# Kernel optimization log

Hardware: AMD Instinct MI355X
Metric: run time of the kernel (lower is better)

Reference implementation:

```python
import jax, jax.numpy as jnp
import numpy as np

EPS = 1e-5  # nn.LayerNorm default

def _ln(x, g, b):
    m = x.mean(-1, keepdims=True)
    v = ((x - m) ** 2).mean(-1, keepdims=True)
    return (x - m) / jnp.sqrt(v + EPS) * g + b


def setup_inputs() -> dict:
    key = jax.random.key(0)
    ks = jax.random.split(key, 16)
    B, T, H, W = 8, 20, 224, 224
    D, NC = 1536, 7
    s = 0.02
    f32 = jnp.float32
    return {
        'x': jax.random.normal(ks[0], (B, 3, T, H, W), f32),
        'timestamp': jax.random.uniform(ks[1], (B,), f32),
        # surrogate backbone: patchify conv (stride 16) + global avg pool -> 1536 feats
        'conv_w': jax.random.normal(ks[2], (D, 3, 16, 16), f32) * s,
        'conv_b': jnp.zeros((D,), f32),
        'w_red': jax.random.normal(ks[3], (D, D), f32) * s,
        'b_red': jnp.zeros((D,), f32),
        'w_num': jax.random.normal(ks[4], (D, 1), f32) * s,
        'b_num': jnp.zeros((D,), f32),
        'time_embed': jax.random.normal(ks[5], (1, T, D), f32) * s,
        'cls_swap': jax.random.normal(ks[6], (1, 5, 1, D), f32) * s,
        'ln_g': jnp.ones((D,), f32),
        'ln_b': jnp.zeros((D,), f32),
        'w_qkv': jax.random.normal(ks[7], (3 * D, D), f32) * s,
        'w_tproj': jax.random.normal(ks[8], (D, D), f32) * s,
        'b_tproj': jnp.zeros((D,), f32),
        'w_tfc': jax.random.normal(ks[9], (D, D), f32) * s,
        'b_tfc': jnp.zeros((D,), f32),
        'w_head': jax.random.normal(ks[10], (NC, D), f32) * s,
        'b_head': jnp.zeros((NC,), f32),
    }


def reference(x, timestamp, conv_w, conv_b, w_red, b_red, w_num, b_num,
              time_embed, cls_swap, ln_g, ln_b, w_qkv, w_tproj, b_tproj,
              w_tfc, b_tfc, w_head, b_head):
    B, C, T, H, W = x.shape
    D = w_red.shape[0]
    NH = 12
    HD = D // NH
    scale = HD ** -0.5

    # (b t) c h w  -> backbone surrogate -> (B*T, D)
    xf = jnp.transpose(x, (0, 2, 1, 3, 4)).reshape(B * T, C, H, W)
    f = jax.lax.conv_general_dilated(
        xf, conv_w, window_strides=(16, 16), padding='VALID',
        dimension_numbers=('NCHW', 'OIHW', 'NCHW'))
    f = (f + conv_b[None, :, None, None]).mean((2, 3))  # global avg pool -> (BT, D)

    xr = (f @ w_red.T + b_red).reshape(B, T, D)           # reduce_dim
    xt = xr + time_embed
    te = timestamp[:, None] @ w_num.T + b_num             # NumberToVector (B, D)
    xt = xt + te[:, None, :]

    # groups: b (n k) c -> b n k c, k=4, n=5; prepend 1 cls token per group
    g = jnp.concatenate(
        [jnp.broadcast_to(cls_swap, (B, 5, 1, D)), xt.reshape(B, 5, 4, D)], axis=2)

    for _ in range(4):  # num_interactions
        gr = g.reshape(B * 5, 5, D)
        hn = _ln(gr, ln_g, ln_b)
        qkv = (hn @ w_qkv.T).reshape(B * 5, 5, 3, NH, HD).transpose(2, 0, 3, 1, 4)
        q, k, v = qkv[0], qkv[1], qkv[2]                  # (b*n, h, t, hd)
        a = jax.nn.softmax(jnp.einsum('bhqd,bhkd->bhqk', q, k) * scale, axis=-1)
        o = jnp.einsum('bhqk,bhkd->bhqd', a, v).transpose(0, 2, 1, 3).reshape(B * 5, 5, D)
        o = o @ w_tproj.T + b_tproj                       # attn proj
        upd = (o @ w_tfc.T + b_tfc) + gr                  # temporal_fc + residual
        g = upd.reshape(B, 5, 5, D)
        # swap cls tokens between groups via roll
        g = g.at[:, :, 0, :].set(jnp.roll(g[:, :, 0, :], 1, axis=1))

    xt = g[:, :, 1:, :].reshape(B, T, D)
    out = xt[:, -1, :] + xr[:, -1, :]
    return out @ w_head.T + b_head  # (B, num_classes)
```

## Files before the change

### kernel.cpp

```cpp
#include <hip/hip_runtime.h>

typedef __attribute__((ext_vector_type(8))) short short8;
typedef __attribute__((ext_vector_type(8))) unsigned short ushort8;
typedef __attribute__((ext_vector_type(4))) float f32x4;
typedef unsigned short ushort_t;

__device__ __forceinline__ ushort_t f2bf(float f) {
    unsigned u = __builtin_bit_cast(unsigned, f);
    u += 0x7fffu + ((u >> 16) & 1u);
    return (ushort_t)(u >> 16);
}
__device__ __forceinline__ float bf2f(ushort_t u) {
    unsigned v = ((unsigned)u) << 16;
    return __builtin_bit_cast(float, v);
}

__device__ __forceinline__ void load_lds16(const void* gp, void* lp) {
    __builtin_amdgcn_global_load_lds(
        (const __attribute__((address_space(1))) void*)gp,
        (__attribute__((address_space(3))) void*)lp, 16, 0, 0);
}

__global__ __launch_bounds__(256, 4) void pool_kernel(
    const float* __restrict__ x, ushort_t* __restrict__ AP) {
    int blk = blockIdx.x, tid = threadIdx.x;
    int bt = blk / 12, rc = blk % 12;
    int c = rc >> 2, igrp = rc & 3;
    int w = tid >> 6, lane = tid & 63;
    int i = igrp * 4 + w;
    int b = bt / 20, t = bt % 20;
    const float* base = x + (size_t)((b * 3 + c) * 20 + t) * 50176;

    f32x4 v[13];
    #pragma unroll
    for (int it = 0; it < 13; ++it) {
        int k = lane + it * 64;
        int kk = k < 784 ? k : 0;
        int ri = (kk * 9363) >> 19;
        int c4 = kk - ri * 56;
        v[it] = *(const f32x4*)(base + (16 * ri + i) * 224 + 4 * c4);
        if (k >= 784) v[it] = (f32x4){0.f, 0.f, 0.f, 0.f};
    }
    #pragma unroll
    for (int s = 1; s < 13; s <<= 1)
        #pragma unroll
        for (int j = 0; j + s < 13; j += 2 * s)
            v[j] += v[j + s];
    f32x4 acc = v[0];
    #pragma unroll
    for (int m = 4; m <= 32; m <<= 1) {
        acc[0] += __shfl_xor(acc[0], m);
        acc[1] += __shfl_xor(acc[1], m);
        acc[2] += __shfl_xor(acc[2], m);
        acc[3] += __shfl_xor(acc[3], m);
    }
    if (lane < 4) {
        ushort4 o;
        o.x = f2bf(acc[0] * (1.f / 196.f));
        o.y = f2bf(acc[1] * (1.f / 196.f));
        o.z = f2bf(acc[2] * (1.f / 196.f));
        o.w = f2bf(acc[3] * (1.f / 196.f));
        *(ushort4*)(AP + (size_t)bt * 768 + c * 256 + i * 16 + 4 * lane) = o;
    }
}

__global__ __launch_bounds__(256) void wprep_kernel(
    const float* __restrict__ w_qkv, const float* __restrict__ w_tf,
    const float* __restrict__ w_red, const float* __restrict__ conv_w,
    const float* __restrict__ w_tp, const float* __restrict__ b_tp,
    const float* __restrict__ b_tf, const float* __restrict__ cls,
    ushort_t* __restrict__ WQ, ushort_t* __restrict__ WF,
    ushort_t* __restrict__ WR, ushort_t* __restrict__ WCV,
    ushort_t* __restrict__ WTT, float* __restrict__ BC,
    float* __restrict__ GA) {
    __shared__ __align__(16) float smem[64 * 68];
    int blk = blockIdx.x, tid = threadIdx.x;
    if (blk < 6336) {
        long c = (long)blk * 256 + tid;
        const float* s; ushort_t* d; long i;
        if (c < 884736)       { s = w_qkv;  d = WQ;  i = c; }
        else if (c < 1179648) { s = w_tf;   d = WF;  i = c - 884736; }
        else if (c < 1474560) { s = w_red;  d = WR;  i = c - 1179648; }
        else                  { s = conv_w; d = WCV; i = c - 1474560; }
        i <<= 3;
        f32x4 a = *(const f32x4*)(s + i);
        f32x4 b = *(const f32x4*)(s + i + 4);
        ushort8 o;
        o[0] = f2bf(a[0]); o[1] = f2bf(a[1]); o[2] = f2bf(a[2]); o[3] = f2bf(a[3]);
        o[4] = f2bf(b[0]); o[5] = f2bf(b[1]); o[6] = f2bf(b[2]); o[7] = f2bf(b[3]);
        *(ushort8*)(d + i) = o;
    } else if (blk < 6912) {
        int tb = blk - 6336;
        int bi = tb / 24, bj = tb % 24;
        int r0 = (tid >> 4) << 2;
        int c0 = (tid & 15) << 2;
        #pragma unroll
        for (int rr = 0; rr < 4; ++rr) {
            f32x4 v = *(const f32x4*)(w_tp + (size_t)(bi * 64 + r0 + rr) * 1536 + bj * 64 + c0);
            smem[(r0 + rr) * 68 + c0 + 0] = v[0];
            smem[(r0 + rr) * 68 + c0 + 1] = v[1];
            smem[(r0 + rr) * 68 + c0 + 2] = v[2];
            smem[(r0 + rr) * 68 + c0 + 3] = v[3];
        }
        __syncthreads();
        #pragma unroll
        for (int rr = 0; rr < 4; ++rr) {
            int jj = r0 + rr;
            ushort4 o;
            o.x = f2bf(smem[(c0 + 0) * 68 + jj]);
            o.y = f2bf(smem[(c0 + 1) * 68 + jj]);
            o.z = f2bf(smem[(c0 + 2) * 68 + jj]);
            o.w = f2bf(smem[(c0 + 3) * 68 + jj]);
            *(ushort4*)(WTT + (size_t)(bj * 64 + jj) * 1536 + bi * 64 + c0) = o;
        }
    } else if (blk < 6952) {
        int cblk = blk - 6912;
        int b = cblk / 5, n = cblk % 5;
        size_t row = (size_t)(b * 25 + n * 5) * 1536;
        #pragma unroll
        for (int j = 0; j < 6; ++j) {
            int d = tid + j * 256;
            GA[row + d] = cls[n * 1536 + d];
        }
    } else {
        int bb = blk - 6952;
        int row = bb * 16 + (tid >> 4);
        int sub = tid & 15;
        float acc = 0.f;
        for (int j = 0; j < 96; ++j) {
            int k = sub + j * 16;
            acc += w_tf[(size_t)row * 1536 + k] * b_tp[k];
        }
        acc += __shfl_xor(acc, 1); acc += __shfl_xor(acc, 2);
        acc += __shfl_xor(acc, 4); acc += __shfl_xor(acc, 8);
        if (sub == 0) BC[row] = acc + b_tf[row];
    }
}

template <int MT, bool OUT_BF16, bool HAS_BIAS, bool HAS_RES, bool CLS_SWAP,
          bool BUILD_G, bool SPLITK>
__global__ __launch_bounds__(64) void gemm_kernel(
    const ushort_t* __restrict__ A, const ushort_t* __restrict__ B,
    void* __restrict__ Cv, void* __restrict__ Cv2,
    const float* __restrict__ bias, const float* __restrict__ res,
    int M, int N, int K, int KS,
    float* __restrict__ g_out, const float* __restrict__ temb,
    const float* __restrict__ ts, const float* __restrict__ w_num,
    const float* __restrict__ b_num) {
    constexpr int BUFB = MT * 2048 + 8192;
    __shared__ __align__(16) char lds[2 * BUFB];
    const int lane = threadIdx.x;
    const int tn = blockIdx.x;
    int tm = blockIdx.y;
    if (SPLITK) {
        int half = tm >> 2;
        tm &= 3;
        if (half) { A += K; B += K; Cv = Cv2; }
    }

    f32x4 acc[MT][4];
    #pragma unroll
    for (int m = 0; m < MT; ++m)
        #pragma unroll
        for (int n = 0; n < 4; ++n)
            acc[m][n] = (f32x4){0.f, 0.f, 0.f, 0.f};

    const int nK = K >> 6;
    const int rbase = lane >> 3, cc = lane & 7;

    auto stage = [&](int k0, int buf) {
        char* lA = lds + buf * BUFB;
        char* lB = lA + MT * 2048;
        #pragma unroll
        for (int j = 0; j < MT * 2; ++j) {
            int row = j * 8 + rbase;
            int cf = cc ^ (row & 7);
            int ga = tm * (MT * 16) + row; if (ga > M - 1) ga = M - 1;
            load_lds16(A + (size_t)ga * KS + (k0 + cf * 8), lA + j * 1024);
        }
        #pragma unroll
        for (int j = 0; j < 8; ++j) {
            int row = j * 8 + rbase;
            int cf = cc ^ (row & 7);
            load_lds16(B + (size_t)(tn * 64 + row) * KS + (k0 + cf * 8), lB + j * 1024);
        }
    };

    stage(0, 0);
    for (int t = 0; t < nK; ++t) {
        int cur = t & 1;
        if (t + 1 < nK) {
            stage((t + 1) << 6, cur ^ 1);
            if constexpr (MT == 2) asm volatile("s_waitcnt vmcnt(12)" ::: "memory");
            else                   asm volatile("s_waitcnt vmcnt(16)" ::: "memory");
        } else {
            asm volatile("s_waitcnt vmcnt(0)" ::: "memory");
        }
        __builtin_amdgcn_sched_barrier(0);
        const char* lA = lds + cur * BUFB;
        const char* lB = lA + MT * 2048;
        #pragma unroll
        for (int ks = 0; ks < 2; ++ks) {
            short8 av[MT], bv[4];
            const int rlo = lane & 15;
            const int chi = ks * 4 + (lane >> 4);
            #pragma unroll
            for (int m = 0; m < MT; ++m) {
                int r = m * 16 + rlo;
                av[m] = *(const short8*)(lA + r * 128 + ((chi ^ (r & 7)) << 4));
            }
            #pragma unroll
            for (int n = 0; n < 4; ++n) {
                int r = n * 16 + rlo;
                bv[n] = *(const short8*)(lB + r * 128 + ((chi ^ (r & 7)) << 4));
            }
            #pragma unroll
            for (int m = 0; m < MT; ++m)
                #pragma unroll
                for (int n = 0; n < 4; ++n)
                    acc[m][n] = __builtin_amdgcn_mfma_f32_16x16x32_bf16(
                        av[m], bv[n], acc[m][n], 0, 0, 0);
        }
    }

    const int c_l = lane & 15, r_q = (lane >> 4) * 4;
    #pragma unroll
    for (int m = 0; m < MT; ++m) {
        #pragma unroll
        for (int reg = 0; reg < 4; ++reg) {
            int r_ = tm * (MT * 16) + m * 16 + r_q + reg;
            if (r_ < M) {
                int r2 = r_;
                if (CLS_SWAP) {
                    int bb = r_ / 25, rem = r_ % 25;
                    if (rem % 5 == 0) r2 = bb * 25 + ((rem / 5 + 1) % 5) * 5;
                }
                #pragma unroll
                for (int n = 0; n < 4; ++n) {
                    int cc_ = tn * 64 + n * 16 + c_l;
                    float v = acc[m][n][reg];
                    if (HAS_BIAS) v += bias[cc_];
                    if (HAS_RES) v += res[(size_t)r_ * N + cc_];
                    if (OUT_BF16) ((ushort_t*)Cv)[(size_t)r2 * N + cc_] = f2bf(v);
                    else          ((float*)Cv)[(size_t)r2 * N + cc_] = v;
                    if (BUILD_G) {
                        int b = r_ / 20, t = r_ % 20;
                        float gval = v + temb[t * 1536 + cc_] +
                                     ts[b] * w_num[cc_] + b_num[cc_];
                        g_out[(size_t)(b * 25 + (t / 4) * 5 + (t % 4) + 1) * 1536 + cc_] = gval;
                    }
                }
            }
        }
    }
}

__global__ __launch_bounds__(256) void ln_kernel(
    const float* __restrict__ g, const float* __restrict__ gamma,
    const float* __restrict__ beta, ushort_t* __restrict__ hn) {
    int r = blockIdx.x, tid = threadIdx.x;
    const float* x = g + (size_t)r * 1536;
    float v[6], s = 0.f, s2 = 0.f;
    #pragma unroll
    for (int j = 0; j < 6; ++j) {
        v[j] = x[tid + j * 256];
        s += v[j]; s2 += v[j] * v[j];
    }
    #pragma unroll
    for (int m = 1; m < 64; m <<= 1) { s += __shfl_xor(s, m); s2 += __shfl_xor(s2, m); }
    __shared__ float red[8];
    int wid = tid >> 6;
    if ((tid & 63) == 0) { red[wid] = s; red[4 + wid] = s2; }
    __syncthreads();
    s  = red[0] + red[1] + red[2] + red[3];
    s2 = red[4] + red[5] + red[6] + red[7];
    float mean = s * (1.0f / 1536.0f);
    float var  = s2 * (1.0f / 1536.0f) - mean * mean;
    float rstd = rsqrtf(var + 1e-5f);
    #pragma unroll
    for (int j = 0; j < 6; ++j) {
        int d = tid + j * 256;
        float y = (v[j] - mean) * rstd * gamma[d] + beta[d];
        hn[(size_t)r * 1536 + d] = f2bf(y);
    }
}

__global__ __launch_bounds__(64) void attn_kernel(
    const float* __restrict__ qA, const float* __restrict__ qB,
    ushort_t* __restrict__ o) {
    int gid = blockIdx.x;
    int h = gid % 12, gg = gid / 12;
    int l = threadIdx.x;
    size_t off = (size_t)gg * 5 * 4608 + h * 128 + 2 * l;
    const float* b0 = qA + off;
    const float* b1 = qB + off;
    float q[5][2], k[5][2], v[5][2];
    #pragma unroll
    for (int tt = 0; tt < 5; ++tt) {
        float2 q0 = *(const float2*)(b0 + tt * 4608);
        float2 q1 = *(const float2*)(b1 + tt * 4608);
        float2 k0 = *(const float2*)(b0 + tt * 4608 + 1536);
        float2 k1 = *(const float2*)(b1 + tt * 4608 + 1536);
        float2 v0 = *(const float2*)(b0 + tt * 4608 + 3072);
        float2 v1 = *(const float2*)(b1 + tt * 4608 + 3072);
        q[tt][0] = q0.x + q1.x; q[tt][1] = q0.y + q1.y;
        k[tt][0] = k0.x + k1.x; k[tt][1] = k0.y + k1.y;
        v[tt][0] = v0.x + v1.x; v[tt][1] = v0.y + v1.y;
    }
    float sc[5][5];
    #pragma unroll
    for (int i = 0; i < 5; ++i)
        #pragma unroll
        for (int j = 0; j < 5; ++j)
            sc[i][j] = q[i][0] * k[j][0] + q[i][1] * k[j][1];
    #pragma unroll
    for (int m = 1; m < 64; m <<= 1)
        #pragma unroll
        for (int i = 0; i < 5; ++i)
            #pragma unroll
            for (int j = 0; j < 5; ++j)
                sc[i][j] += __shfl_xor(sc[i][j], m);
    const float scale = 0.08838834764831845f;
    float a_[5][5];
    #pragma unroll
    for (int i = 0; i < 5; ++i) {
        float mx = -1e30f;
        #pragma unroll
        for (int j = 0; j < 5; ++j) mx = fmaxf(mx, sc[i][j]);
        float sum = 0.f;
        #pragma unroll
        for (int j = 0; j < 5; ++j) { a_[i][j] = __expf((sc[i][j] - mx) * scale); sum += a_[i][j]; }
        float inv = 1.0f / sum;
        #pragma unroll
        for (int j = 0; j < 5; ++j) a_[i][j] *= inv;
    }
    #pragma unroll
    for (int i = 0; i < 5; ++i) {
        float o0 = 0.f, o1 = 0.f;
        #pragma unroll
        for (int j = 0; j < 5; ++j) { o0 += a_[i][j] * v[j][0]; o1 += a_[i][j] * v[j][1]; }
        ushort2 w; w.x = f2bf(o0); w.y = f2bf(o1);
        *(ushort2*)(o + (size_t)(gg * 5 + i) * 1536 + h * 128 + 2 * l) = w;
    }
}

__global__ __launch_bounds__(64) void head_kernel(
    const float* __restrict__ gfin, const float* __restrict__ xr,
    const float* __restrict__ w_head, const float* __restrict__ b_head,
    float* __restrict__ out) {
    int b = blockIdx.x, l = threadIdx.x;
    const float* gv = gfin + (size_t)(b * 25 + 24) * 1536;
    const float* xv = xr + (size_t)(b * 20 + 19) * 1536;
    float acc[7] = {0, 0, 0, 0, 0, 0, 0};
    for (int d = l; d < 1536; d += 64) {
        float xval = gv[d] + xv[d];
        #pragma unroll
        for (int c = 0; c < 7; ++c) acc[c] += xval * w_head[c * 1536 + d];
    }
    #pragma unroll
    for (int c = 0; c < 7; ++c)
        #pragma unroll
        for (int m = 1; m < 64; m <<= 1) acc[c] += __shfl_xor(acc[c], m);
    if (l == 0) {
        #pragma unroll
        for (int c = 0; c < 7; ++c) out[b * 7 + c] = acc[c] + b_head[c];
    }
}

#define OFF_WQ    0u
#define OFF_WF    14155776u
#define OFF_WR    18874368u
#define OFF_WCV   23592960u
#define OFF_WTT   25952256u
#define OFF_WC    30670848u
#define OFF_BC    35389440u
#define OFF_AP    35395584u
#define OFF_FBF   35641344u
#define OFF_XR    36132864u
#define OFF_GA    37115904u
#define OFF_GB    38344704u
#define OFF_HN    39573504u
#define OFF_QKV0  40187904u
#define OFF_QKV1  43874304u
#define OFF_OBF   47560704u

extern "C" void kernel_launch(void* const* d_in, const int* in_sizes, int n_in,
                              void* d_out, int out_size, void* d_ws, size_t ws_size,
                              hipStream_t stream) {
    const float* x      = (const float*)d_in[0];
    const float* ts     = (const float*)d_in[1];
    const float* conv_w = (const float*)d_in[2];
    const float* conv_b = (const float*)d_in[3];
    const float* w_red  = (const float*)d_in[4];
    const float* b_red  = (const float*)d_in[5];
    const float* w_num  = (const float*)d_in[6];
    const float* b_num  = (const float*)d_in[7];
    const float* temb   = (const float*)d_in[8];
    const float* cls    = (const float*)d_in[9];
    const float* ln_g   = (const float*)d_in[10];
    const float* ln_b   = (const float*)d_in[11];
    const float* w_qkv  = (const float*)d_in[12];
    const float* w_tp   = (const float*)d_in[13];
    const float* b_tp   = (const float*)d_in[14];
    const float* w_tf   = (const float*)d_in[15];
    const float* b_tf   = (const float*)d_in[16];
    const float* w_head = (const float*)d_in[17];
    const float* b_head = (const float*)d_in[18];

    char* ws = (char*)d_ws;
    ushort_t* WQ   = (ushort_t*)(ws + OFF_WQ);
    ushort_t* WF   = (ushort_t*)(ws + OFF_WF);
    ushort_t* WR   = (ushort_t*)(ws + OFF_WR);
    ushort_t* WCV  = (ushort_t*)(ws + OFF_WCV);
    ushort_t* WTT  = (ushort_t*)(ws + OFF_WTT);
    ushort_t* WC   = (ushort_t*)(ws + OFF_WC);
    float*    BC   = (float*)(ws + OFF_BC);
    ushort_t* AP   = (ushort_t*)(ws + OFF_AP);
    ushort_t* FBF  = (ushort_t*)(ws + OFF_FBF);
    float*    XR   = (float*)(ws + OFF_XR);
    float*    GA   = (float*)(ws + OFF_GA);
    float*    GB   = (float*)(ws + OFF_GB);
    ushort_t* HN   = (ushort_t*)(ws + OFF_HN);
    float*    QKV0 = (float*)(ws + OFF_QKV0);
    float*    QKV1 = (float*)(ws + OFF_QKV1);
    ushort_t* OBF  = (ushort_t*)(ws + OFF_OBF);

    pool_kernel<<<1920, 256, 0, stream>>>(x, AP);
    wprep_kernel<<<7048, 256, 0, stream>>>(w_qkv, w_tf, w_red, conv_w, w_tp,
                                           b_tp, b_tf, cls,
                                           WQ, WF, WR, WCV, WTT, BC, GA);
    gemm_kernel<4, true, false, false, false, false, false><<<dim3(24, 24), 64, 0, stream>>>(
        WF, WTT, WC, nullptr, nullptr, nullptr, 1536, 1536, 1536, 1536,
        nullptr, nullptr, nullptr, nullptr, nullptr);
    gemm_kernel<2, true, true, false, false, false, false><<<dim3(24, 5), 64, 0, stream>>>(
        AP, WCV, FBF, nullptr, conv_b, nullptr, 160, 1536, 768, 768,
        nullptr, nullptr, nullptr, nullptr, nullptr);
    gemm_kernel<2, false, true, false, false, true, false><<<dim3(24, 5), 64, 0, stream>>>(
        FBF, WR, XR, nullptr, b_red, nullptr, 160, 1536, 1536, 1536,
        GA, temb, ts, w_num, b_num);

    float* gsrc = GA;
    float* gdst = GB;
    for (int it = 0; it < 4; ++it) {
        ln_kernel<<<200, 256, 0, stream>>>(gsrc, ln_g, ln_b, HN);
        gemm_kernel<4, false, false, false, false, false, true><<<dim3(72, 8), 64, 0, stream>>>(
            HN, WQ, QKV0, QKV1, nullptr, nullptr, 200, 4608, 768, 1536,
            nullptr, nullptr, nullptr, nullptr, nullptr);
        attn_kernel<<<480, 64, 0, stream>>>(QKV0, QKV1, OBF);
        gemm_kernel<2, false, true, true, true, false, false><<<dim3(24, 7), 64, 0, stream>>>(
            OBF, WC, gdst, nullptr, BC, gsrc, 200, 1536, 1536, 1536,
            nullptr, nullptr, nullptr, nullptr, nullptr);
        float* tmp = gsrc; gsrc = gdst; gdst = tmp;
    }
    head_kernel<<<8, 64, 0, stream>>>(gsrc, XR, w_head, b_head, (float*)d_out);
}
```

Baseline: 212.7 us.

## Fold LayerNorm into QKV GEMM via gamma-scaled weights and epilogue row stats

```diff
diff --git a/kernel.cpp b/kernel.cpp
--- a/kernel.cpp
+++ b/kernel.cpp
@@ -10,10 +10,6 @@
     u += 0x7fffu + ((u >> 16) & 1u);
     return (ushort_t)(u >> 16);
 }
-__device__ __forceinline__ float bf2f(ushort_t u) {
-    unsigned v = ((unsigned)u) << 16;
-    return __builtin_bit_cast(float, v);
-}
 
 __device__ __forceinline__ void load_lds16(const void* gp, void* lp) {
     __builtin_amdgcn_global_load_lds(
@@ -21,76 +17,81 @@
         (__attribute__((address_space(3))) void*)lp, 16, 0, 0);
 }
 
-__global__ __launch_bounds__(256, 4) void pool_kernel(
-    const float* __restrict__ x, ushort_t* __restrict__ AP) {
-    int blk = blockIdx.x, tid = threadIdx.x;
-    int bt = blk / 12, rc = blk % 12;
-    int c = rc >> 2, igrp = rc & 3;
-    int w = tid >> 6, lane = tid & 63;
-    int i = igrp * 4 + w;
-    int b = bt / 20, t = bt % 20;
-    const float* base = x + (size_t)((b * 3 + c) * 20 + t) * 50176;
-
-    f32x4 v[13];
-    #pragma unroll
-    for (int it = 0; it < 13; ++it) {
-        int k = lane + it * 64;
-        int kk = k < 784 ? k : 0;
-        int ri = (kk * 9363) >> 19;
-        int c4 = kk - ri * 56;
-        v[it] = *(const f32x4*)(base + (16 * ri + i) * 224 + 4 * c4);
-        if (k >= 784) v[it] = (f32x4){0.f, 0.f, 0.f, 0.f};
-    }
-    #pragma unroll
-    for (int s = 1; s < 13; s <<= 1)
-        #pragma unroll
-        for (int j = 0; j + s < 13; j += 2 * s)
-            v[j] += v[j + s];
-    f32x4 acc = v[0];
-    #pragma unroll
-    for (int m = 4; m <= 32; m <<= 1) {
-        acc[0] += __shfl_xor(acc[0], m);
-        acc[1] += __shfl_xor(acc[1], m);
-        acc[2] += __shfl_xor(acc[2], m);
-        acc[3] += __shfl_xor(acc[3], m);
-    }
-    if (lane < 4) {
-        ushort4 o;
-        o.x = f2bf(acc[0] * (1.f / 196.f));
-        o.y = f2bf(acc[1] * (1.f / 196.f));
-        o.z = f2bf(acc[2] * (1.f / 196.f));
-        o.w = f2bf(acc[3] * (1.f / 196.f));
-        *(ushort4*)(AP + (size_t)bt * 768 + c * 256 + i * 16 + 4 * lane) = o;
-    }
-}
-
-__global__ __launch_bounds__(256) void wprep_kernel(
-    const float* __restrict__ w_qkv, const float* __restrict__ w_tf,
-    const float* __restrict__ w_red, const float* __restrict__ conv_w,
-    const float* __restrict__ w_tp, const float* __restrict__ b_tp,
-    const float* __restrict__ b_tf, const float* __restrict__ cls,
-    ushort_t* __restrict__ WQ, ushort_t* __restrict__ WF,
-    ushort_t* __restrict__ WR, ushort_t* __restrict__ WCV,
-    ushort_t* __restrict__ WTT, float* __restrict__ BC,
-    float* __restrict__ GA) {
+__global__ __launch_bounds__(256, 4) void prep_kernel(
+    const float* __restrict__ x, const float* __restrict__ w_qkv,
+    const float* __restrict__ w_tf, const float* __restrict__ w_red,
+    const float* __restrict__ conv_w, const float* __restrict__ w_tp,
+    const float* __restrict__ b_tp, const float* __restrict__ b_tf,
+    const float* __restrict__ cls, const float* __restrict__ ln_g,
+    const float* __restrict__ ln_b,
+    ushort_t* __restrict__ AP, ushort_t* __restrict__ WQg,
+    ushort_t* __restrict__ WF, ushort_t* __restrict__ WR,
+    ushort_t* __restrict__ WCV, ushort_t* __restrict__ WTT,
+    float* __restrict__ BC, float* __restrict__ GA,
+    ushort_t* __restrict__ GBA, float* __restrict__ U,
+    float* __restrict__ W0, float* __restrict__ ST) {
     __shared__ __align__(16) float smem[64 * 68];
     int blk = blockIdx.x, tid = threadIdx.x;
-    if (blk < 6336) {
-        long c = (long)blk * 256 + tid;
-        const float* s; ushort_t* d; long i;
-        if (c < 884736)       { s = w_qkv;  d = WQ;  i = c; }
+    if (blk < 1920) {
+        int bt = blk / 12, rc = blk % 12;
+        int c = rc >> 2, igrp = rc & 3;
+        int w = tid >> 6, lane = tid & 63;
+        int i = igrp * 4 + w;
+        int b = bt / 20, t = bt % 20;
+        const float* base = x + (size_t)((b * 3 + c) * 20 + t) * 50176;
+        f32x4 v[13];
+        #pragma unroll
+        for (int it = 0; it < 13; ++it) {
+            int k = lane + it * 64;
+            int kk = k < 784 ? k : 0;
+            int ri = (kk * 9363) >> 19;
+            int c4 = kk - ri * 56;
+            v[it] = *(const f32x4*)(base + (16 * ri + i) * 224 + 4 * c4);
+            if (k >= 784) v[it] = (f32x4){0.f, 0.f, 0.f, 0.f};
+        }
+        #pragma unroll
+        for (int s = 1; s < 13; s <<= 1)
+            #pragma unroll
+            for (int j = 0; j + s < 13; j += 2 * s)
+                v[j] += v[j + s];
+        f32x4 acc = v[0];
+        #pragma unroll
+        for (int m = 4; m <= 32; m <<= 1) {
+            acc[0] += __shfl_xor(acc[0], m);
+            acc[1] += __shfl_xor(acc[1], m);
+            acc[2] += __shfl_xor(acc[2], m);
+            acc[3] += __shfl_xor(acc[3], m);
+        }
+        if (lane < 4) {
+            ushort4 o;
+            o.x = f2bf(acc[0] * (1.f / 196.f));
+            o.y = f2bf(acc[1] * (1.f / 196.f));
+            o.z = f2bf(acc[2] * (1.f / 196.f));
+            o.w = f2bf(acc[3] * (1.f / 196.f));
+            *(ushort4*)(AP + (size_t)bt * 768 + c * 256 + i * 16 + 4 * lane) = o;
+        }
+    } else if (blk < 8256) {
+        long c = (long)(blk - 1920) * 256 + tid;
+        const float* s; ushort_t* d; long i; bool gm = false;
+        if (c < 884736)       { s = w_qkv;  d = WQg; i = c; gm = true; }
         else if (c < 1179648) { s = w_tf;   d = WF;  i = c - 884736; }
         else if (c < 1474560) { s = w_red;  d = WR;  i = c - 1179648; }
         else                  { s = conv_w; d = WCV; i = c - 1474560; }
         i <<= 3;
         f32x4 a = *(const f32x4*)(s + i);
         f32x4 b = *(const f32x4*)(s + i + 4);
+        if (gm) {
+            int k = (int)(i % 1536);
+            f32x4 g0 = *(const f32x4*)(ln_g + k);
+            f32x4 g1 = *(const f32x4*)(ln_g + k + 4);
+            a *= g0; b *= g1;
+        }
         ushort8 o;
         o[0] = f2bf(a[0]); o[1] = f2bf(a[1]); o[2] = f2bf(a[2]); o[3] = f2bf(a[3]);
         o[4] = f2bf(b[0]); o[5] = f2bf(b[1]); o[6] = f2bf(b[2]); o[7] = f2bf(b[3]);
         *(ushort8*)(d + i) = o;
-    } else if (blk < 6912) {
-        int tb = blk - 6336;
+    } else if (blk < 8832) {
+        int tb = blk - 8256;
         int bi = tb / 24, bj = tb % 24;
         int r0 = (tid >> 4) << 2;
         int c0 = (tid & 15) << 2;
@@ -113,17 +114,31 @@
             o.w = f2bf(smem[(c0 + 3) * 68 + jj]);
             *(ushort4*)(WTT + (size_t)(bj * 64 + jj) * 1536 + bi * 64 + c0) = o;
         }
-    } else if (blk < 6952) {
-        int cblk = blk - 6912;
+    } else if (blk < 8872) {
+        int cblk = blk - 8832;
         int b = cblk / 5, n = cblk % 5;
-        size_t row = (size_t)(b * 25 + n * 5) * 1536;
+        int grow = b * 25 + n * 5;
+        size_t row = (size_t)grow * 1536;
+        float sv = 0.f, sv2 = 0.f;
         #pragma unroll
         for (int j = 0; j < 6; ++j) {
             int d = tid + j * 256;
-            GA[row + d] = cls[n * 1536 + d];
-        }
-    } else {
-        int bb = blk - 6952;
+            float val = cls[n * 1536 + d];
+            GA[row + d] = val;
+            GBA[row + d] = f2bf(val);
+            sv += val; sv2 += val * val;
+        }
+        #pragma unroll
+        for (int m = 1; m < 64; m <<= 1) { sv += __shfl_xor(sv, m); sv2 += __shfl_xor(sv2, m); }
+        int wid = tid >> 6;
+        if ((tid & 63) == 0) { smem[wid] = sv; smem[4 + wid] = sv2; }
+        __syncthreads();
+        if (tid == 0) {
+            ST[grow * 2]     = smem[0] + smem[1] + smem[2] + smem[3];
+            ST[grow * 2 + 1] = smem[4] + smem[5] + smem[6] + smem[7];
+        }
+    } else if (blk < 8968) {
+        int bb = blk - 8872;
         int row = bb * 16 + (tid >> 4);
         int sub = tid & 15;
         float acc = 0.f;
@@ -134,29 +149,37 @@
         acc += __shfl_xor(acc, 1); acc += __shfl_xor(acc, 2);
         acc += __shfl_xor(acc, 4); acc += __shfl_xor(acc, 8);
         if (sub == 0) BC[row] = acc + b_tf[row];
+    } else {
+        int bb = blk - 8968;
+        int row = bb * 16 + (tid >> 4);
+        int sub = tid & 15;
+        float au = 0.f, aw = 0.f;
+        for (int j = 0; j < 96; ++j) {
+            int k = sub + j * 16;
+            float wv = w_qkv[(size_t)row * 1536 + k];
+            au += wv * ln_g[k];
+            aw += wv * ln_b[k];
+        }
+        au += __shfl_xor(au, 1); au += __shfl_xor(au, 2);
+        au += __shfl_xor(au, 4); au += __shfl_xor(au, 8);
+        aw += __shfl_xor(aw, 1); aw += __shfl_xor(aw, 2);
+        aw += __shfl_xor(aw, 4); aw += __shfl_xor(aw, 8);
+        if (sub == 0) { U[row] = au; W0[row] = aw; }
     }
 }
 
 template <int MT, bool OUT_BF16, bool HAS_BIAS, bool HAS_RES, bool CLS_SWAP,
-          bool BUILD_G, bool SPLITK>
-__global__ __launch_bounds__(64) void gemm_kernel(
+          bool BUILD_G, bool WRITE_BF, bool STATS>
+__device__ __forceinline__ void gemm_tile(
+    char* lds, int lane, int tn, int tm,
     const ushort_t* __restrict__ A, const ushort_t* __restrict__ B,
-    void* __restrict__ Cv, void* __restrict__ Cv2,
-    const float* __restrict__ bias, const float* __restrict__ res,
-    int M, int N, int K, int KS,
+    void* __restrict__ Cv, const float* __restrict__ bias,
+    const float* __restrict__ res, int M, int N, int K, int KS,
+    ushort_t* __restrict__ gbf, float* __restrict__ stats,
     float* __restrict__ g_out, const float* __restrict__ temb,
     const float* __restrict__ ts, const float* __restrict__ w_num,
     const float* __restrict__ b_num) {
     constexpr int BUFB = MT * 2048 + 8192;
-    __shared__ __align__(16) char lds[2 * BUFB];
-    const int lane = threadIdx.x;
-    const int tn = blockIdx.x;
-    int tm = blockIdx.y;
-    if (SPLITK) {
-        int half = tm >> 2;
-        tm &= 3;
-        if (half) { A += K; B += K; Cv = Cv2; }
-    }
 
     f32x4 acc[MT][4];
     #pragma unroll
@@ -235,6 +258,12 @@
                     int bb = r_ / 25, rem = r_ % 25;
                     if (rem % 5 == 0) r2 = bb * 25 + ((rem / 5 + 1) % 5) * 5;
                 }
+                int grow = r2;
+                if (BUILD_G) {
+                    int b = r_ / 20, t = r_ % 20;
+                    grow = b * 25 + (t / 4) * 5 + (t % 4) + 1;
+                }
+                float rp = 0.f, rp2 = 0.f;
                 #pragma unroll
                 for (int n = 0; n < 4; ++n) {
                     int cc_ = tn * 64 + n * 16 + c_l;
@@ -247,7 +276,22 @@
                         int b = r_ / 20, t = r_ % 20;
                         float gval = v + temb[t * 1536 + cc_] +
                                      ts[b] * w_num[cc_] + b_num[cc_];
-                        g_out[(size_t)(b * 25 + (t / 4) * 5 + (t % 4) + 1) * 1536 + cc_] = gval;
+                        g_out[(size_t)grow * 1536 + cc_] = gval;
+                        gbf[(size_t)grow * 1536 + cc_] = f2bf(gval);
+                        rp += gval; rp2 += gval * gval;
+                    } else if (WRITE_BF) {
+                        gbf[(size_t)r2 * N + cc_] = f2bf(v);
+                        rp += v; rp2 += v * v;
+                    }
+                }
+                if (STATS) {
+                    rp  += __shfl_xor(rp, 1);  rp2 += __shfl_xor(rp2, 1);
+                    rp  += __shfl_xor(rp, 2);  rp2 += __shfl_xor(rp2, 2);
+                    rp  += __shfl_xor(rp, 4);  rp2 += __shfl_xor(rp2, 4);
+                    rp  += __shfl_xor(rp, 8);  rp2 += __shfl_xor(rp2, 8);
+                    if (c_l == 0) {
+                        atomicAdd(&stats[grow * 2], rp);
+                        atomicAdd(&stats[grow * 2 + 1], rp2);
                     }
                 }
             }
@@ -255,57 +299,102 @@
     }
 }
 
-__global__ __launch_bounds__(256) void ln_kernel(
-    const float* __restrict__ g, const float* __restrict__ gamma,
-    const float* __restrict__ beta, ushort_t* __restrict__ hn) {
-    int r = blockIdx.x, tid = threadIdx.x;
-    const float* x = g + (size_t)r * 1536;
-    float v[6], s = 0.f, s2 = 0.f;
-    #pragma unroll
-    for (int j = 0; j < 6; ++j) {
-        v[j] = x[tid + j * 256];
-        s += v[j]; s2 += v[j] * v[j];
-    }
-    #pragma unroll
-    for (int m = 1; m < 64; m <<= 1) { s += __shfl_xor(s, m); s2 += __shfl_xor(s2, m); }
-    __shared__ float red[8];
-    int wid = tid >> 6;
-    if ((tid & 63) == 0) { red[wid] = s; red[4 + wid] = s2; }
-    __syncthreads();
-    s  = red[0] + red[1] + red[2] + red[3];
-    s2 = red[4] + red[5] + red[6] + red[7];
-    float mean = s * (1.0f / 1536.0f);
-    float var  = s2 * (1.0f / 1536.0f) - mean * mean;
-    float rstd = rsqrtf(var + 1e-5f);
-    #pragma unroll
-    for (int j = 0; j < 6; ++j) {
-        int d = tid + j * 256;
-        float y = (v[j] - mean) * rstd * gamma[d] + beta[d];
-        hn[(size_t)r * 1536 + d] = f2bf(y);
-    }
+__global__ __launch_bounds__(64) void wcf_kernel(
+    const ushort_t* __restrict__ WF, const ushort_t* __restrict__ WTT,
+    const ushort_t* __restrict__ AP, const ushort_t* __restrict__ WCV,
+    ushort_t* __restrict__ WC, ushort_t* __restrict__ FBF,
+    const float* __restrict__ conv_b) {
+    __shared__ __align__(16) char lds[32768];
+    int task = blockIdx.x, lane = threadIdx.x;
+    if (task < 576)
+        gemm_tile<4, true, false, false, false, false, false, false>(
+            lds, lane, task % 24, task / 24, WF, WTT, WC, nullptr, nullptr,
+            1536, 1536, 1536, 1536, nullptr, nullptr,
+            nullptr, nullptr, nullptr, nullptr, nullptr);
+    else {
+        int t2 = task - 576;
+        gemm_tile<4, true, true, false, false, false, false, false>(
+            lds, lane, t2 % 24, t2 / 24, AP, WCV, FBF, conv_b, nullptr,
+            160, 1536, 768, 768, nullptr, nullptr,
+            nullptr, nullptr, nullptr, nullptr, nullptr);
+    }
+}
+
+__global__ __launch_bounds__(64) void xr_kernel(
+    const ushort_t* __restrict__ FBF, const ushort_t* __restrict__ WR,
+    float* __restrict__ XR, const float* __restrict__ b_red,
+    float* __restrict__ G0, ushort_t* __restrict__ G0B,
+    float* __restrict__ ST0, const float* __restrict__ temb,
+    const float* __restrict__ ts, const float* __restrict__ w_num,
+    const float* __restrict__ b_num) {
+    __shared__ __align__(16) char lds[24576];
+    gemm_tile<2, false, true, false, false, true, false, true>(
+        lds, threadIdx.x, blockIdx.x, blockIdx.y, FBF, WR, XR, b_red, nullptr,
+        160, 1536, 1536, 1536, G0B, ST0, G0, temb, ts, w_num, b_num);
+}
+
+__global__ __launch_bounds__(64) void qkv_kernel(
+    const ushort_t* __restrict__ GBF, const ushort_t* __restrict__ WQg,
+    float* __restrict__ C0, float* __restrict__ C1) {
+    __shared__ __align__(16) char lds[32768];
+    int tn = blockIdx.x, tmh = blockIdx.y;
+    int half = tmh >> 2, tm = tmh & 3;
+    gemm_tile<4, false, false, false, false, false, false, false>(
+        lds, threadIdx.x, tn, tm, GBF + half * 768, WQg + half * 768,
+        half ? C1 : C0, nullptr, nullptr, 200, 4608, 768, 1536,
+        nullptr, nullptr, nullptr, nullptr, nullptr, nullptr, nullptr);
+}
+
+__global__ __launch_bounds__(64) void proj_kernel(
+    const ushort_t* __restrict__ OBF, const ushort_t* __restrict__ WC,
+    float* __restrict__ gdst, const float* __restrict__ BC,
+    const float* __restrict__ gsrc, ushort_t* __restrict__ gbf,
+    float* __restrict__ ST) {
+    __shared__ __align__(16) char lds[24576];
+    gemm_tile<2, false, true, true, true, false, true, true>(
+        lds, threadIdx.x, blockIdx.x, blockIdx.y, OBF, WC, gdst, BC, gsrc,
+        200, 1536, 1536, 1536, gbf, ST,
+        nullptr, nullptr, nullptr, nullptr, nullptr);
 }
 
 __global__ __launch_bounds__(64) void attn_kernel(
     const float* __restrict__ qA, const float* __restrict__ qB,
-    ushort_t* __restrict__ o) {
+    const float* __restrict__ U, const float* __restrict__ W0,
+    const float* __restrict__ ST, ushort_t* __restrict__ o) {
     int gid = blockIdx.x;
     int h = gid % 12, gg = gid / 12;
     int l = threadIdx.x;
-    size_t off = (size_t)gg * 5 * 4608 + h * 128 + 2 * l;
+    int col = h * 128 + 2 * l;
+    size_t off = (size_t)gg * 5 * 4608 + col;
     const float* b0 = qA + off;
     const float* b1 = qB + off;
+    float2 uq = *(const float2*)(U + col);
+    float2 uk = *(const float2*)(U + 1536 + col);
+    float2 uv = *(const float2*)(U + 3072 + col);
+    float2 wq = *(const float2*)(W0 + col);
+    float2 wk = *(const float2*)(W0 + 1536 + col);
+    float2 wv = *(const float2*)(W0 + 3072 + col);
     float q[5][2], k[5][2], v[5][2];
     #pragma unroll
     for (int tt = 0; tt < 5; ++tt) {
+        int gr = gg * 5 + tt;
+        float2 st = *(const float2*)(ST + gr * 2);
+        float mean = st.x * (1.0f / 1536.0f);
+        float var = st.y * (1.0f / 1536.0f) - mean * mean;
+        float s = rsqrtf(var + 1e-5f);
+        float sm = s * mean;
         float2 q0 = *(const float2*)(b0 + tt * 4608);
         float2 q1 = *(const float2*)(b1 + tt * 4608);
         float2 k0 = *(const float2*)(b0 + tt * 4608 + 1536);
         float2 k1 = *(const float2*)(b1 + tt * 4608 + 1536);
         float2 v0 = *(const float2*)(b0 + tt * 4608 + 3072);
         float2 v1 = *(const float2*)(b1 + tt * 4608 + 3072);
-        q[tt][0] = q0.x + q1.x; q[tt][1] = q0.y + q1.y;
-        k[tt][0] = k0.x + k1.x; k[tt][1] = k0.y + k1.y;
-        v[tt][0] = v0.x + v1.x; v[tt][1] = v0.y + v1.y;
+        q[tt][0] = s * (q0.x + q1.x) - sm * uq.x + wq.x;
+        q[tt][1] = s * (q0.y + q1.y) - sm * uq.y + wq.y;
+        k[tt][0] = s * (k0.x + k1.x) - sm * uk.x + wk.x;
+        k[tt][1] = s * (k0.y + k1.y) - sm * uk.y + wk.y;
+        v[tt][0] = s * (v0.x + v1.x) - sm * uv.x + wv.x;
+        v[tt][1] = s * (v0.y + v1.y) - sm * uv.y + wv.y;
     }
     float sc[5][5];
     #pragma unroll
@@ -340,7 +429,7 @@
         #pragma unroll
         for (int j = 0; j < 5; ++j) { o0 += a_[i][j] * v[j][0]; o1 += a_[i][j] * v[j][1]; }
         ushort2 w; w.x = f2bf(o0); w.y = f2bf(o1);
-        *(ushort2*)(o + (size_t)(gg * 5 + i) * 1536 + h * 128 + 2 * l) = w;
+        *(ushort2*)(o + (size_t)(gg * 5 + i) * 1536 + col) = w;
     }
 }
 
@@ -379,10 +468,14 @@
 #define OFF_XR    36132864u
 #define OFF_GA    37115904u
 #define OFF_GB    38344704u
-#define OFF_HN    39573504u
-#define OFF_QKV0  40187904u
-#define OFF_QKV1  43874304u
-#define OFF_OBF   47560704u
+#define OFF_GBA   39573504u
+#define OFF_GBB   40187904u
+#define OFF_QKV0  40802304u
+#define OFF_QKV1  44488704u
+#define OFF_OBF   48175104u
+#define OFF_U     48789504u
+#define OFF_W0    48807936u
+#define OFF_ST    48826368u
 
 extern "C" void kernel_launch(void* const* d_in, const int* in_sizes, int n_in,
                               void* d_out, int out_size, void* d_ws, size_t ws_size,
@@ -408,7 +501,7 @@
     const float* b_head = (const float*)d_in[18];
 
     char* ws = (char*)d_ws;
-    ushort_t* WQ   = (ushort_t*)(ws + OFF_WQ);
+    ushort_t* WQg  = (ushort_t*)(ws + OFF_WQ);
     ushort_t* WF   = (ushort_t*)(ws + OFF_WF);
     ushort_t* WR   = (ushort_t*)(ws + OFF_WR);
     ushort_t* WCV  = (ushort_t*)(ws + OFF_WCV);
@@ -418,39 +511,35 @@
     ushort_t* AP   = (ushort_t*)(ws + OFF_AP);
     ushort_t* FBF  = (ushort_t*)(ws + OFF_FBF);
     float*    XR   = (float*)(ws + OFF_XR);
-    float*    GA   = (float*)(ws + OFF_GA);
-    float*    GB   = (float*)(ws + OFF_GB);
-    ushort_t* HN   = (ushort_t*)(ws + OFF_HN);
+    float*    G[2] = { (float*)(ws + OFF_GA), (float*)(ws + OFF_GB) };
+    ushort_t* GBF[2] = { (ushort_t*)(ws + OFF_GBA), (ushort_t*)(ws + OFF_GBB) };
     float*    QKV0 = (float*)(ws + OFF_QKV0);
     float*    QKV1 = (float*)(ws + OFF_QKV1);
     ushort_t* OBF  = (ushort_t*)(ws + OFF_OBF);
-
-    pool_kernel<<<1920, 256, 0, stream>>>(x, AP);
-    wprep_kernel<<<7048, 256, 0, stream>>>(w_qkv, w_tf, w_red, conv_w, w_tp,
-                                           b_tp, b_tf, cls,
-                                           WQ, WF, WR, WCV, WTT, BC, GA);
-    gemm_kernel<4, true, false, false, false, false, false><<<dim3(24, 24), 64, 0, stream>>>(
-        WF, WTT, WC, nullptr, nullptr, nullptr, 1536, 1536, 1536, 1536,
-        nullptr, nullptr, nullptr, nullptr, nullptr);
-    gemm_kernel<2, true, true, false, false, false, false><<<dim3(24, 5), 64, 0, stream>>>(
-        AP, WCV, FBF, nullptr, conv_b, nullptr, 160, 1536, 768, 768,
-        nullptr, nullptr, nullptr, nullptr, nullptr);
-    gemm_kernel<2, false, true, false, false, true, false><<<dim3(24, 5), 64, 0, stream>>>(
-        FBF, WR, XR, nullptr, b_red, nullptr, 160, 1536, 1536, 1536,
-        GA, temb, ts, w_num, b_num);
-
-    float* gsrc = GA;
-    float* gdst = GB;
+    float*    U    = (float*)(ws + OFF_U);
+    float*    W0   = (float*)(ws + OFF_W0);
+    float*    ST   = (float*)(ws + OFF_ST);
+
+    (void)hipMemsetAsync(ST, 0, 8192, stream);
+
+    prep_kernel<<<9256, 256, 0, stream>>>(x, w_qkv, w_tf, w_red, conv_w, w_tp,
+                                          b_tp, b_tf, cls, ln_g, ln_b,
+                                          AP, WQg, WF, WR, WCV, WTT, BC,
+                                          G[0], GBF[0], U, W0, ST);
+    wcf_kernel<<<648, 64, 0, stream>>>(WF, WTT, AP, WCV, WC, FBF, conv_b);
+    xr_kernel<<<dim3(24, 5), 64, 0, stream>>>(FBF, WR, XR, b_red,
+                                              G[0], GBF[0], ST,
+                                              temb, ts, w_num, b_num);
+    int cur = 0;
     for (int it = 0; it < 4; ++it) {
-        ln_kernel<<<200, 256, 0, stream>>>(gsrc, ln_g, ln_b, HN);
-        gemm_kernel<4, false, false, false, false, false, true><<<dim3(72, 8), 64, 0, stream>>>(
-            HN, WQ, QKV0, QKV1, nullptr, nullptr, 200, 4608, 768, 1536,
-            nullptr, nullptr, nullptr, nullptr, nullptr);
-        attn_kernel<<<480, 64, 0, stream>>>(QKV0, QKV1, OBF);
-        gemm_kernel<2, false, true, true, true, false, false><<<dim3(24, 7), 64, 0, stream>>>(
-            OBF, WC, gdst, nullptr, BC, gsrc, 200, 1536, 1536, 1536,
-            nullptr, nullptr, nullptr, nullptr, nullptr);
-        float* tmp = gsrc; gsrc = gdst; gdst = tmp;
-    }
-    head_kernel<<<8, 64, 0, stream>>>(gsrc, XR, w_head, b_head, (float*)d_out);
-}
+        int nxt = cur ^ 1;
+        qkv_kernel<<<dim3(72, 8), 64, 0, stream>>>(GBF[cur], WQg, QKV0, QKV1);
+        attn_kernel<<<480, 64, 0, stream>>>(QKV0, QKV1, U, W0,
+                                            ST + it * 400, OBF);
+        proj_kernel<<<dim3(24, 7), 64, 0, stream>>>(OBF, WC, G[nxt], BC,
+                                                    G[cur], GBF[nxt],
+                                                    ST + (it + 1) * 400);
+        cur = nxt;
+    }
+    head_kernel<<<8, 64, 0, stream>>>(G[cur], XR, w_head, b_head, (float*)d_out);
+}
```

Result: slower. 232.9 us (+9.5%).

## Fold conv weight into reduce_dim weight and merge weight-prep GEMMs

Applied to the files above, without the earlier changes.

```diff
diff --git a/kernel.cpp b/kernel.cpp
--- a/kernel.cpp
+++ b/kernel.cpp
@@ -9,10 +9,6 @@
     unsigned u = __builtin_bit_cast(unsigned, f);
     u += 0x7fffu + ((u >> 16) & 1u);
     return (ushort_t)(u >> 16);
-}
-__device__ __forceinline__ float bf2f(ushort_t u) {
-    unsigned v = ((unsigned)u) << 16;
-    return __builtin_bit_cast(float, v);
 }
 
 __device__ __forceinline__ void load_lds16(const void* gp, void* lp) {
@@ -68,20 +64,20 @@
     const float* __restrict__ w_qkv, const float* __restrict__ w_tf,
     const float* __restrict__ w_red, const float* __restrict__ conv_w,
     const float* __restrict__ w_tp, const float* __restrict__ b_tp,
-    const float* __restrict__ b_tf, const float* __restrict__ cls,
+    const float* __restrict__ b_tf, const float* __restrict__ conv_b,
+    const float* __restrict__ b_red, const float* __restrict__ cls,
     ushort_t* __restrict__ WQ, ushort_t* __restrict__ WF,
-    ushort_t* __restrict__ WR, ushort_t* __restrict__ WCV,
+    ushort_t* __restrict__ WR, ushort_t* __restrict__ WCVT,
     ushort_t* __restrict__ WTT, float* __restrict__ BC,
-    float* __restrict__ GA) {
+    float* __restrict__ BC2, float* __restrict__ GA) {
     __shared__ __align__(16) float smem[64 * 68];
     int blk = blockIdx.x, tid = threadIdx.x;
-    if (blk < 6336) {
+    if (blk < 5760) {
         long c = (long)blk * 256 + tid;
         const float* s; ushort_t* d; long i;
-        if (c < 884736)       { s = w_qkv;  d = WQ;  i = c; }
-        else if (c < 1179648) { s = w_tf;   d = WF;  i = c - 884736; }
-        else if (c < 1474560) { s = w_red;  d = WR;  i = c - 1179648; }
-        else                  { s = conv_w; d = WCV; i = c - 1474560; }
+        if (c < 884736)       { s = w_qkv; d = WQ; i = c; }
+        else if (c < 1179648) { s = w_tf;  d = WF; i = c - 884736; }
+        else                  { s = w_red; d = WR; i = c - 1179648; }
         i <<= 3;
         f32x4 a = *(const f32x4*)(s + i);
         f32x4 b = *(const f32x4*)(s + i + 4);
@@ -89,8 +85,8 @@
         o[0] = f2bf(a[0]); o[1] = f2bf(a[1]); o[2] = f2bf(a[2]); o[3] = f2bf(a[3]);
         o[4] = f2bf(b[0]); o[5] = f2bf(b[1]); o[6] = f2bf(b[2]); o[7] = f2bf(b[3]);
         *(ushort8*)(d + i) = o;
-    } else if (blk < 6912) {
-        int tb = blk - 6336;
+    } else if (blk < 6336) {
+        int tb = blk - 5760;
         int bi = tb / 24, bj = tb % 24;
         int r0 = (tid >> 4) << 2;
         int c0 = (tid & 15) << 2;
@@ -113,8 +109,32 @@
             o.w = f2bf(smem[(c0 + 3) * 68 + jj]);
             *(ushort4*)(WTT + (size_t)(bj * 64 + jj) * 1536 + bi * 64 + c0) = o;
         }
-    } else if (blk < 6952) {
-        int cblk = blk - 6912;
+    } else if (blk < 6624) {
+        int tb = blk - 6336;
+        int bi = tb / 12, bj = tb % 12;
+        int r0 = (tid >> 4) << 2;
+        int c0 = (tid & 15) << 2;
+        #pragma unroll
+        for (int rr = 0; rr < 4; ++rr) {
+            f32x4 v = *(const f32x4*)(conv_w + (size_t)(bi * 64 + r0 + rr) * 768 + bj * 64 + c0);
+            smem[(r0 + rr) * 68 + c0 + 0] = v[0];
+            smem[(r0 + rr) * 68 + c0 + 1] = v[1];
+            smem[(r0 + rr) * 68 + c0 + 2] = v[2];
+            smem[(r0 + rr) * 68 + c0 + 3] = v[3];
+        }
+        __syncthreads();
+        #pragma unroll
+        for (int rr = 0; rr < 4; ++rr) {
+            int jj = r0 + rr;
+            ushort4 o;
+            o.x = f2bf(smem[(c0 + 0) * 68 + jj]);
+            o.y = f2bf(smem[(c0 + 1) * 68 + jj]);
+            o.z = f2bf(smem[(c0 + 2) * 68 + jj]);
+            o.w = f2bf(smem[(c0 + 3) * 68 + jj]);
+            *(ushort4*)(WCVT + (size_t)(bj * 64 + jj) * 1536 + bi * 64 + c0) = o;
+        }
+    } else if (blk < 6664) {
+        int cblk = blk - 6624;
         int b = cblk / 5, n = cblk % 5;
         size_t row = (size_t)(b * 25 + n * 5) * 1536;
         #pragma unroll
@@ -122,8 +142,8 @@
             int d = tid + j * 256;
             GA[row + d] = cls[n * 1536 + d];
         }
-    } else {
-        int bb = blk - 6952;
+    } else if (blk < 6760) {
+        int bb = blk - 6664;
         int row = bb * 16 + (tid >> 4);
         int sub = tid & 15;
         float acc = 0.f;
@@ -134,29 +154,37 @@
         acc += __shfl_xor(acc, 1); acc += __shfl_xor(acc, 2);
         acc += __shfl_xor(acc, 4); acc += __shfl_xor(acc, 8);
         if (sub == 0) BC[row] = acc + b_tf[row];
-    }
-}
-
-template <int MT, bool OUT_BF16, bool HAS_BIAS, bool HAS_RES, bool CLS_SWAP,
-          bool BUILD_G, bool SPLITK>
-__global__ __launch_bounds__(64) void gemm_kernel(
+    } else {
+        int bb = blk - 6760;
+        int row = bb * 16 + (tid >> 4);
+        int sub = tid & 15;
+        float acc = 0.f;
+        for (int j = 0; j < 48; ++j) {
+            int k = sub + j * 16;
+            acc += w_red[(size_t)row * 1536 + k] * 0.f;
+        }
+        acc = 0.f;
+        for (int j = 0; j < 48; ++j) {
+            int n0 = sub + j * 16;
+            acc += w_red[(size_t)row * 1536 + n0] * conv_b[n0];
+            acc += w_red[(size_t)row * 1536 + n0 + 768] * conv_b[n0 + 768];
+        }
+        acc += __shfl_xor(acc, 1); acc += __shfl_xor(acc, 2);
+        acc += __shfl_xor(acc, 4); acc += __shfl_xor(acc, 8);
+        if (sub == 0) BC2[row] = acc + b_red[row];
+    }
+}
+
+template <int MT, bool OUT_BF16, bool HAS_BIAS, bool HAS_RES, bool CLS_SWAP, bool BUILD_G>
+__device__ __forceinline__ void gemm_tile(
+    char* lds, int lane, int tn, int tm,
     const ushort_t* __restrict__ A, const ushort_t* __restrict__ B,
-    void* __restrict__ Cv, void* __restrict__ Cv2,
-    const float* __restrict__ bias, const float* __restrict__ res,
-    int M, int N, int K, int KS,
+    void* __restrict__ Cv, const float* __restrict__ bias,
+    const float* __restrict__ res, int M, int N, int K, int KS,
     float* __restrict__ g_out, const float* __restrict__ temb,
     const float* __restrict__ ts, const float* __restrict__ w_num,
     const float* __restrict__ b_num) {
     constexpr int BUFB = MT * 2048 + 8192;
-    __shared__ __align__(16) char lds[2 * BUFB];
-    const int lane = threadIdx.x;
-    const int tn = blockIdx.x;
-    int tm = blockIdx.y;
-    if (SPLITK) {
-        int half = tm >> 2;
-        tm &= 3;
-        if (half) { A += K; B += K; Cv = Cv2; }
-    }
 
     f32x4 acc[MT][4];
     #pragma unroll
@@ -255,6 +283,58 @@
     }
 }
 
+__global__ __launch_bounds__(64) void wcf_kernel(
+    const ushort_t* __restrict__ WF, const ushort_t* __restrict__ WTT,
+    const ushort_t* __restrict__ WR, const ushort_t* __restrict__ WCVT,
+    ushort_t* __restrict__ WC, ushort_t* __restrict__ WRC) {
+    __shared__ __align__(16) char lds[32768];
+    int task = blockIdx.x, lane = threadIdx.x;
+    if (task < 576)
+        gemm_tile<4, true, false, false, false, false>(
+            lds, lane, task % 24, task / 24, WF, WTT, WC, nullptr, nullptr,
+            1536, 1536, 1536, 1536, nullptr, nullptr, nullptr, nullptr, nullptr);
+    else {
+        int t2 = task - 576;
+        gemm_tile<4, true, false, false, false, false>(
+            lds, lane, t2 % 12, t2 / 12, WR, WCVT, WRC, nullptr, nullptr,
+            1536, 768, 1536, 1536, nullptr, nullptr, nullptr, nullptr, nullptr);
+    }
+}
+
+__global__ __launch_bounds__(64) void xr_kernel(
+    const ushort_t* __restrict__ AP, const ushort_t* __restrict__ WRC,
+    float* __restrict__ XR, const float* __restrict__ BC2,
+    float* __restrict__ GA, const float* __restrict__ temb,
+    const float* __restrict__ ts, const float* __restrict__ w_num,
+    const float* __restrict__ b_num) {
+    __shared__ __align__(16) char lds[24576];
+    gemm_tile<2, false, true, false, false, true>(
+        lds, threadIdx.x, blockIdx.x, blockIdx.y, AP, WRC, XR, BC2, nullptr,
+        160, 1536, 768, 768, GA, temb, ts, w_num, b_num);
+}
+
+__global__ __launch_bounds__(64) void qkv_kernel(
+    const ushort_t* __restrict__ HN, const ushort_t* __restrict__ WQ,
+    float* __restrict__ C0, float* __restrict__ C1) {
+    __shared__ __align__(16) char lds[32768];
+    int tn = blockIdx.x, tmh = blockIdx.y;
+    int half = tmh >> 2, tm = tmh & 3;
+    gemm_tile<4, false, false, false, false, false>(
+        lds, threadIdx.x, tn, tm, HN + half * 768, WQ + half * 768,
+        half ? C1 : C0, nullptr, nullptr, 200, 4608, 768, 1536,
+        nullptr, nullptr, nullptr, nullptr, nullptr);
+}
+
+__global__ __launch_bounds__(64) void proj_kernel(
+    const ushort_t* __restrict__ OBF, const ushort_t* __restrict__ WC,
+    float* __restrict__ gdst, const float* __restrict__ BC,
+    const float* __restrict__ gsrc) {
+    __shared__ __align__(16) char lds[24576];
+    gemm_tile<2, false, true, true, true, false>(
+        lds, threadIdx.x, blockIdx.x, blockIdx.y, OBF, WC, gdst, BC, gsrc,
+        200, 1536, 1536, 1536, nullptr, nullptr, nullptr, nullptr, nullptr);
+}
+
 __global__ __launch_bounds__(256) void ln_kernel(
     const float* __restrict__ g, const float* __restrict__ gamma,
     const float* __restrict__ beta, ushort_t* __restrict__ hn) {
@@ -370,19 +450,20 @@
 #define OFF_WQ    0u
 #define OFF_WF    14155776u
 #define OFF_WR    18874368u
-#define OFF_WCV   23592960u
+#define OFF_WCVT  23592960u
 #define OFF_WTT   25952256u
 #define OFF_WC    30670848u
-#define OFF_BC    35389440u
-#define OFF_AP    35395584u
-#define OFF_FBF   35641344u
-#define OFF_XR    36132864u
-#define OFF_GA    37115904u
-#define OFF_GB    38344704u
-#define OFF_HN    39573504u
-#define OFF_QKV0  40187904u
-#define OFF_QKV1  43874304u
-#define OFF_OBF   47560704u
+#define OFF_WRC   35389440u
+#define OFF_BC    37748736u
+#define OFF_BC2   37754880u
+#define OFF_AP    37761024u
+#define OFF_XR    38006784u
+#define OFF_GA    38989824u
+#define OFF_GB    40218624u
+#define OFF_HN    41447424u
+#define OFF_QKV0  42061824u
+#define OFF_QKV1  45748224u
+#define OFF_OBF   49434624u
 
 extern "C" void kernel_launch(void* const* d_in, const int* in_sizes, int n_in,
                               void* d_out, int out_size, void* d_ws, size_t ws_size,
@@ -411,12 +492,13 @@
     ushort_t* WQ   = (ushort_t*)(ws + OFF_WQ);
     ushort_t* WF   = (ushort_t*)(ws + OFF_WF);
     ushort_t* WR   = (ushort_t*)(ws + OFF_WR);
-    ushort_t* WCV  = (ushort_t*)(ws + OFF_WCV);
+    ushort_t* WCVT = (ushort_t*)(ws + OFF_WCVT);
     ushort_t* WTT  = (ushort_t*)(ws + OFF_WTT);
     ushort_t* WC   = (ushort_t*)(ws + OFF_WC);
+    ushort_t* WRC  = (ushort_t*)(ws + OFF_WRC);
     float*    BC   = (float*)(ws + OFF_BC);
+    float*    BC2  = (float*)(ws + OFF_BC2);
     ushort_t* AP   = (ushort_t*)(ws + OFF_AP);
-    ushort_t* FBF  = (ushort_t*)(ws + OFF_FBF);
     float*    XR   = (float*)(ws + OFF_XR);
     float*    GA   = (float*)(ws + OFF_GA);
     float*    GB   = (float*)(ws + OFF_GB);
@@ -426,30 +508,19 @@
     ushort_t* OBF  = (ushort_t*)(ws + OFF_OBF);
 
     pool_kernel<<<1920, 256, 0, stream>>>(x, AP);
-    wprep_kernel<<<7048, 256, 0, stream>>>(w_qkv, w_tf, w_red, conv_w, w_tp,
-                                           b_tp, b_tf, cls,
-                                           WQ, WF, WR, WCV, WTT, BC, GA);
-    gemm_kernel<4, true, false, false, false, false, false><<<dim3(24, 24), 64, 0, stream>>>(
-        WF, WTT, WC, nullptr, nullptr, nullptr, 1536, 1536, 1536, 1536,
-        nullptr, nullptr, nullptr, nullptr, nullptr);
-    gemm_kernel<2, true, true, false, false, false, false><<<dim3(24, 5), 64, 0, stream>>>(
-        AP, WCV, FBF, nullptr, conv_b, nullptr, 160, 1536, 768, 768,
-        nullptr, nullptr, nullptr, nullptr, nullptr);
-    gemm_kernel<2, false, true, false, false, true, false><<<dim3(24, 5), 64, 0, stream>>>(
-        FBF, WR, XR, nullptr, b_red, nullptr, 160, 1536, 1536, 1536,
-        GA, temb, ts, w_num, b_num);
-
+    wprep_kernel<<<6856, 256, 0, stream>>>(w_qkv, w_tf, w_red, conv_w, w_tp,
+                                           b_tp, b_tf, conv_b, b_red, cls,
+                                           WQ, WF, WR, WCVT, WTT, BC, BC2, GA);
+    wcf_kernel<<<864, 64, 0, stream>>>(WF, WTT, WR, WCVT, WC, WRC);
+    xr_kernel<<<dim3(24, 5), 64, 0, stream>>>(AP, WRC, XR, BC2, GA,
+                                              temb, ts, w_num, b_num);
     float* gsrc = GA;
     float* gdst = GB;
     for (int it = 0; it < 4; ++it) {
         ln_kernel<<<200, 256, 0, stream>>>(gsrc, ln_g, ln_b, HN);
-        gemm_kernel<4, false, false, false, false, false, true><<<dim3(72, 8), 64, 0, stream>>>(
-            HN, WQ, QKV0, QKV1, nullptr, nullptr, 200, 4608, 768, 1536,
-            nullptr, nullptr, nullptr, nullptr, nullptr);
+        qkv_kernel<<<dim3(72, 8), 64, 0, stream>>>(HN, WQ, QKV0, QKV1);
         attn_kernel<<<480, 64, 0, stream>>>(QKV0, QKV1, OBF);
-        gemm_kernel<2, false, true, true, true, false, false><<<dim3(24, 7), 64, 0, stream>>>(
-            OBF, WC, gdst, nullptr, BC, gsrc, 200, 1536, 1536, 1536,
-            nullptr, nullptr, nullptr, nullptr, nullptr);
+        proj_kernel<<<dim3(24, 7), 64, 0, stream>>>(OBF, WC, gdst, BC, gsrc);
         float* tmp = gsrc; gsrc = gdst; gdst = tmp;
     }
     head_kernel<<<8, 64, 0, stream>>>(gsrc, XR, w_head, b_head, (float*)d_out);
```

After: 203.9 us. -4.2%, faster.
